# Kernel tuning notes

Measured on AMD Instinct MI355X. Metric: run time of the kernel, lower is better.

## Reference

```python
import jax, jax.numpy as jnp
import numpy as np

B, T, N_EMBD, HEAD = 8, 2048, 1024, 64
NEG_INF = -1e30  # stand-in for float('-inf'), safe under fp16/bf16 after where


def setup_inputs() -> dict:
    key = jax.random.key(0)
    k0, k1, k2, k3 = jax.random.split(key, 4)
    idx = jax.random.normal(k0, (B, T, N_EMBD), dtype=jnp.float32)
    # nn.Linear weights have shape (out_features, in_features)
    Wk = jax.random.normal(k1, (HEAD, N_EMBD), dtype=jnp.float32) * 0.02
    Wq = jax.random.normal(k2, (HEAD, N_EMBD), dtype=jnp.float32) * 0.02
    Wv = jax.random.normal(k3, (HEAD, N_EMBD), dtype=jnp.float32) * 0.02
    return {"idx": idx, "Wk": Wk, "Wq": Wq, "Wv": Wv}


def reference(idx, Wk, Wq, Wv):
    # idx: [B,T,C]; W*: [H,C] (torch Linear layout, y = x @ W.T)
    Tn = idx.shape[1]
    k = jnp.einsum('btc,hc->bth', idx, Wk)
    q = jnp.einsum('btc,hc->bth', idx, Wq)
    v = jnp.einsum('btc,hc->bth', idx, Wv)
    # NOTE: original has NO 1/sqrt(head_size) scaling
    wei = jnp.einsum('bth,bsh->bts', q, k)  # [B,T,T]
    causal = jnp.tril(jnp.ones((Tn, Tn), dtype=bool))  # keep where tril != 0
    wei = jnp.where(causal[None, :, :], wei, NEG_INF)
    # NOTE: original softmaxes over dim=1 (query axis), not the last axis
    wei = jax.nn.softmax(wei, axis=1)
    out = jnp.einsum('bts,bsh->bth', wei, v)  # [B,T,H]
    return out
```

## Files before the change

kernel.cpp:

```cpp
#include <hip/hip_runtime.h>


typedef __attribute__((ext_vector_type(8))) short bf16x8;
typedef __attribute__((ext_vector_type(4))) float f32x4;
typedef unsigned short u16;

#define MFMA(a, b, c) __builtin_amdgcn_mfma_f32_16x16x32_bf16((a), (b), (c), 0, 0, 0)

__device__ __forceinline__ u16 f2bf(float x) {
    unsigned u = __float_as_uint(x);
    u += 0x7fff + ((u >> 16) & 1);
    return (u16)(u >> 16);
}
__device__ __forceinline__ float bf2f(u16 h) {
    return __uint_as_float(((unsigned)h) << 16);
}

#define WH_OFF 0u
#define WL_OFF (WH_OFF + 192u*1024u*2u)
#define QH_OFF (WL_OFF + 192u*1024u*2u)
#define QL_OFF (QH_OFF + 8u*2048u*64u*2u)
#define KH_OFF (QL_OFF + 8u*2048u*64u*2u)
#define KL_OFF (KH_OFF + 8u*2048u*64u*2u)
#define VT_OFF (KL_OFF + 8u*2048u*64u*2u)
#define DD_OFF (VT_OFF + 8u*2048u*64u*2u)

__global__ __launch_bounds__(128) void wsplit_kernel(
    const float* __restrict__ Wk, const float* __restrict__ Wq,
    const float* __restrict__ Wv, u16* __restrict__ FWH, u16* __restrict__ FWL)
{
    const int n = blockIdx.x;
    const int nblk = n >> 4, lr = n & 15;
    const float* src = (n < 64) ? (Wq + (long)n * 1024)
                     : (n < 128) ? (Wk + (long)(n - 64) * 1024)
                                 : (Wv + (long)(n - 128) * 1024);
    const int f = threadIdx.x;
    const int kc = f >> 2, q = f & 3;
    const float4 f0 = *(const float4*)&src[kc * 32 + q * 8];
    const float4 f1 = *(const float4*)&src[kc * 32 + q * 8 + 4];
    const float vs[8] = {f0.x, f0.y, f0.z, f0.w, f1.x, f1.y, f1.z, f1.w};
    bf16x8 hv, lv;
    #pragma unroll
    for (int j = 0; j < 8; ++j) {
        const u16 h = f2bf(vs[j]);
        hv[j] = (short)h;
        lv[j] = (short)f2bf(vs[j] - bf2f(h));
    }
    const long o = ((long)(nblk * 32 + kc) * 64 + q * 16 + lr) * 8;
    *(bf16x8*)&FWH[o] = hv;
    *(bf16x8*)&FWL[o] = lv;
}

__global__ __launch_bounds__(512, 2) void qkv_kernel(
    const float* __restrict__ idx, const u16* __restrict__ FWH, const u16* __restrict__ FWL,
    u16* __restrict__ QH, u16* __restrict__ QL,
    u16* __restrict__ KH, u16* __restrict__ KL, u16* __restrict__ VT)
{
    __shared__ u16 a_l[2][64 * 136];
    const int tid = threadIdx.x;
    const int w = tid >> 6, lr = tid & 15, quad = (tid >> 4) & 3;
    const int lane = tid & 63;
    const int r0 = blockIdx.x * 64;
    const int b = r0 >> 11, t0 = r0 & 2047;
    const int m0 = (w & 1) * 32;
    const int nbb = (w >> 1) * 3;
    const int sr = tid >> 3, sc = (tid & 7) * 8;
    const float* arow = &idx[(long)(r0 + sr) * 1024 + sc];

    f32x4 acc[2][3] = {};
    float4 pf0, pf1;

    pf0 = *(const float4*)(arow);
    pf1 = *(const float4*)(arow + 4);
    {
        const float vs[8] = {pf0.x, pf0.y, pf0.z, pf0.w, pf1.x, pf1.y, pf1.z, pf1.w};
        bf16x8 hv, lv;
        #pragma unroll
        for (int j = 0; j < 8; ++j) {
            const u16 h = f2bf(vs[j]);
            hv[j] = (short)h;
            lv[j] = (short)f2bf(vs[j] - bf2f(h));
        }
        *(bf16x8*)&a_l[0][sr * 136 + sc]      = hv;
        *(bf16x8*)&a_l[0][sr * 136 + 64 + sc] = lv;
    }
    __syncthreads();

    int p = 0;
    for (int it = 0; it < 16; ++it) {
        const int c0 = it * 64;
        if (it < 15) {
            pf0 = *(const float4*)(arow + c0 + 64);
            pf1 = *(const float4*)(arow + c0 + 68);
        }

        bf16x8 AH[2][2], AL[2][2];
        #pragma unroll
        for (int mi = 0; mi < 2; ++mi) {
            const int ar = (m0 + mi * 16 + lr) * 136 + quad * 8;
            AH[mi][0] = *(const bf16x8*)&a_l[p][ar];
            AH[mi][1] = *(const bf16x8*)&a_l[p][ar + 32];
            AL[mi][0] = *(const bf16x8*)&a_l[p][ar + 64];
            AL[mi][1] = *(const bf16x8*)&a_l[p][ar + 96];
        }

        #pragma unroll
        for (int nf = 0; nf < 3; ++nf) {
            const long base = ((long)((nbb + nf) * 32 + 2 * it) * 64 + lane) * 8;
            const bf16x8 bh0 = *(const bf16x8*)&FWH[base];
            const bf16x8 bh1 = *(const bf16x8*)&FWH[base + 512];
            const bf16x8 bl0 = *(const bf16x8*)&FWL[base];
            const bf16x8 bl1 = *(const bf16x8*)&FWL[base + 512];
            #pragma unroll
            for (int mi = 0; mi < 2; ++mi) {
                f32x4 c = acc[mi][nf];
                c = MFMA(AH[mi][0], bh0, c);
                c = MFMA(AL[mi][0], bh0, c);
                c = MFMA(AH[mi][0], bl0, c);
                c = MFMA(AH[mi][1], bh1, c);
                c = MFMA(AL[mi][1], bh1, c);
                c = MFMA(AH[mi][1], bl1, c);
                acc[mi][nf] = c;
            }
        }

        if (it < 15) {
            const float vs[8] = {pf0.x, pf0.y, pf0.z, pf0.w, pf1.x, pf1.y, pf1.z, pf1.w};
            bf16x8 hv, lv;
            #pragma unroll
            for (int j = 0; j < 8; ++j) {
                const u16 h = f2bf(vs[j]);
                hv[j] = (short)h;
                lv[j] = (short)f2bf(vs[j] - bf2f(h));
            }
            *(bf16x8*)&a_l[p ^ 1][sr * 136 + sc]      = hv;
            *(bf16x8*)&a_l[p ^ 1][sr * 136 + 64 + sc] = lv;
            __syncthreads();
            p ^= 1;
        }
    }

    #pragma unroll
    for (int mi = 0; mi < 2; ++mi) {
        const int tb = t0 + m0 + mi * 16 + quad * 4;
        #pragma unroll
        for (int nf = 0; nf < 3; ++nf) {
            const int n = (nbb + nf) * 16 + lr;
            const f32x4 a = acc[mi][nf];
            if (n < 128) {
                u16* Hd = (n < 64) ? QH : KH;
                u16* Ld = (n < 64) ? QL : KL;
                const int h = n & 63;
                #pragma unroll
                for (int r = 0; r < 4; ++r) {
                    const float v = a[r];
                    const u16 hi = f2bf(v);
                    const u16 lo = f2bf(v - bf2f(hi));
                    const long o = (long)(b * 2048 + tb + r) * 64 + h;
                    Hd[o] = hi; Ld[o] = lo;
                }
            } else {
                *(ushort4*)&VT[(long)(b * 64 + n - 128) * 2048 + tb] =
                    make_ushort4(f2bf(a[0]), f2bf(a[1]), f2bf(a[2]), f2bf(a[3]));
            }
        }
    }
}

__global__ __launch_bounds__(256) void stats_kernel(
    const u16* __restrict__ QH, const u16* __restrict__ QL,
    const u16* __restrict__ KH, const u16* __restrict__ KL,
    float* __restrict__ D)
{
    __shared__ u16 kt[64 * 136];
    __shared__ u16 qt[64 * 136];
    __shared__ float red[4][64];
    const int tid = threadIdx.x;
    const int w = tid >> 6, lr = tid & 15, quad = (tid >> 4) & 3;
    const int b = blockIdx.y;
    int x = blockIdx.x, i = 0;
    for (;;) { const int nc = (39 - i) >> 3; if (x < nc) break; x -= nc; ++i; }
    const int c = x;
    const int s0 = i * 64;

    #pragma unroll
    for (int it = 0; it < 2; ++it) {
        const int e = it * 256 + tid;
        const int s = e >> 3, c8 = e & 7;
        const long g = (long)(b * 2048 + s0 + s) * 64 + 8 * c8;
        *(float4*)&kt[s * 136 + 8 * c8]      = *(const float4*)&KH[g];
        *(float4*)&kt[s * 136 + 64 + 8 * c8] = *(const float4*)&KL[g];
    }

    float dsum[4] = {0.f, 0.f, 0.f, 0.f};
    const int ar = (w * 16 + lr) * 136;
    const int jt1 = min(i + 8 * c + 8, 32);
    for (int jt = i + 8 * c; jt < jt1; ++jt) {
        __syncthreads();
        #pragma unroll
        for (int it = 0; it < 2; ++it) {
            const int e = it * 256 + tid;
            const int t = e >> 3, c8 = e & 7;
            const long g = (long)(b * 2048 + jt * 64 + t) * 64 + 8 * c8;
            *(float4*)&qt[t * 136 + 8 * c8]      = *(const float4*)&QH[g];
            *(float4*)&qt[t * 136 + 64 + 8 * c8] = *(const float4*)&QL[g];
        }
        __syncthreads();

        const bf16x8 ah0 = *(const bf16x8*)&qt[ar + quad * 8];
        const bf16x8 al0 = *(const bf16x8*)&qt[ar + 64 + quad * 8];
        const bf16x8 ah1 = *(const bf16x8*)&qt[ar + 32 + quad * 8];
        const bf16x8 al1 = *(const bf16x8*)&qt[ar + 96 + quad * 8];
        #pragma unroll
        for (int nf = 0; nf < 4; ++nf) {
            const int br = (nf * 16 + lr) * 136;
            f32x4 cc = {};
            const bf16x8 bh0 = *(const bf16x8*)&kt[br + quad * 8];
            const bf16x8 bl0 = *(const bf16x8*)&kt[br + 64 + quad * 8];
            cc = MFMA(ah0, bh0, cc); cc = MFMA(ah0, bl0, cc); cc = MFMA(al0, bh0, cc);
            const bf16x8 bh1 = *(const bf16x8*)&kt[br + 32 + quad * 8];
            const bf16x8 bl1 = *(const bf16x8*)&kt[br + 96 + quad * 8];
            cc = MFMA(ah1, bh1, cc); cc = MFMA(ah1, bl1, cc); cc = MFMA(al1, bh1, cc);

            if (jt > i) {
                dsum[nf] += __expf(cc[0]) + __expf(cc[1]) + __expf(cc[2]) + __expf(cc[3]);
            } else {
                const int sl = nf * 16 + lr;
                #pragma unroll
                for (int r = 0; r < 4; ++r) {
                    const int tl = w * 16 + quad * 4 + r;
                    if (tl >= sl) dsum[nf] += __expf(cc[r]);
                }
            }
        }
    }

    #pragma unroll
    for (int nf = 0; nf < 4; ++nf) {
        dsum[nf] += __shfl_xor(dsum[nf], 16);
        dsum[nf] += __shfl_xor(dsum[nf], 32);
    }
    if (quad == 0) {
        #pragma unroll
        for (int nf = 0; nf < 4; ++nf) red[w][nf * 16 + lr] = dsum[nf];
    }
    __syncthreads();
    if (tid < 64)
        atomicAdd(&D[b * 2048 + s0 + tid],
                  red[0][tid] + red[1][tid] + red[2][tid] + red[3][tid]);
}

__global__ __launch_bounds__(256) void out_kernel(
    const u16* __restrict__ QH, const u16* __restrict__ QL,
    const u16* __restrict__ KH, const u16* __restrict__ KL,
    const u16* __restrict__ VT, const float* __restrict__ D,
    float* __restrict__ out)
{
    __shared__ u16 qt[64 * 136];
    __shared__ u16 kt[64 * 136];
    __shared__ u16 vt[64 * 72];
    __shared__ u16 wa[64 * 72];
    __shared__ float rdt[64];
    const int tid = threadIdx.x;
    const int w = tid >> 6, lr = tid & 15, quad = (tid >> 4) & 3;
    const int b = blockIdx.y;
    int x = blockIdx.x, i = 0;
    for (;;) { const int nc = (i + 8) >> 3; if (x < nc) break; x -= nc; ++i; }
    const int c = x;
    const int t0 = i * 64;

    #pragma unroll
    for (int it = 0; it < 2; ++it) {
        const int e = it * 256 + tid;
        const int t = e >> 3, c8 = e & 7;
        const long g = (long)(b * 2048 + t0 + t) * 64 + 8 * c8;
        *(float4*)&qt[t * 136 + 8 * c8]      = *(const float4*)&QH[g];
        *(float4*)&qt[t * 136 + 64 + 8 * c8] = *(const float4*)&QL[g];
    }

    f32x4 oacc[4] = {};
    const int ar = (w * 16 + lr) * 136;
    const int js1 = min(8 * c + 8, i + 1);
    for (int js = 8 * c; js < js1; ++js) {
        const int s0 = js * 64;
        __syncthreads();
        #pragma unroll
        for (int it = 0; it < 2; ++it) {
            const int e = it * 256 + tid;
            const int s = e >> 3, c8 = e & 7;
            const long g = (long)(b * 2048 + s0 + s) * 64 + 8 * c8;
            *(float4*)&kt[s * 136 + 8 * c8]      = *(const float4*)&KH[g];
            *(float4*)&kt[s * 136 + 64 + 8 * c8] = *(const float4*)&KL[g];
        }
        #pragma unroll
        for (int it = 0; it < 2; ++it) {
            const int e = it * 256 + tid;
            const int h = e >> 3, c8 = e & 7;
            *(float4*)&vt[h * 72 + 8 * c8] =
                *(const float4*)&VT[(long)(b * 64 + h) * 2048 + s0 + 8 * c8];
        }
        if (tid < 64) rdt[tid] = 1.0f / D[b * 2048 + s0 + tid];
        __syncthreads();

        const bf16x8 ah0 = *(const bf16x8*)&qt[ar + quad * 8];
        const bf16x8 al0 = *(const bf16x8*)&qt[ar + 64 + quad * 8];
        const bf16x8 ah1 = *(const bf16x8*)&qt[ar + 32 + quad * 8];
        const bf16x8 al1 = *(const bf16x8*)&qt[ar + 96 + quad * 8];
        const bool diag = (js == i);
        #pragma unroll
        for (int nf = 0; nf < 4; ++nf) {
            const int br = (nf * 16 + lr) * 136;
            f32x4 cc = {};
            const bf16x8 bh0 = *(const bf16x8*)&kt[br + quad * 8];
            const bf16x8 bl0 = *(const bf16x8*)&kt[br + 64 + quad * 8];
            cc = MFMA(ah0, bh0, cc); cc = MFMA(ah0, bl0, cc); cc = MFMA(al0, bh0, cc);
            const bf16x8 bh1 = *(const bf16x8*)&kt[br + 32 + quad * 8];
            const bf16x8 bl1 = *(const bf16x8*)&kt[br + 96 + quad * 8];
            cc = MFMA(ah1, bh1, cc); cc = MFMA(ah1, bl1, cc); cc = MFMA(al1, bh1, cc);

            const int sl = nf * 16 + lr;
            const float rv = rdt[sl];
            #pragma unroll
            for (int r = 0; r < 4; ++r) {
                const int tl = w * 16 + quad * 4 + r;
                float wgt = __expf(cc[r]) * rv;
                if (diag && tl < sl) wgt = 0.f;
                wa[tl * 72 + sl] = f2bf(wgt);
            }
        }
        #pragma unroll
        for (int kk = 0; kk < 2; ++kk) {
            const bf16x8 av = *(const bf16x8*)&wa[(w * 16 + lr) * 72 + kk * 32 + quad * 8];
            #pragma unroll
            for (int nf = 0; nf < 4; ++nf) {
                const bf16x8 bv = *(const bf16x8*)&vt[(nf * 16 + lr) * 72 + kk * 32 + quad * 8];
                oacc[nf] = MFMA(av, bv, oacc[nf]);
            }
        }
    }

    const bool single = (i < 8);
    #pragma unroll
    for (int nf = 0; nf < 4; ++nf) {
        const int h = nf * 16 + lr;
        #pragma unroll
        for (int r = 0; r < 4; ++r) {
            const int t = t0 + w * 16 + quad * 4 + r;
            const long o = (long)(b * 2048 + t) * 64 + h;
            if (single) out[o] = oacc[nf][r];
            else        atomicAdd(&out[o], oacc[nf][r]);
        }
    }
}

extern "C" void kernel_launch(void* const* d_in, const int* in_sizes, int n_in,
                              void* d_out, int out_size, void* d_ws, size_t ws_size,
                              hipStream_t stream)
{
    const float* idx = (const float*)d_in[0];
    const float* Wk  = (const float*)d_in[1];
    const float* Wq  = (const float*)d_in[2];
    const float* Wv  = (const float*)d_in[3];
    char* ws = (char*)d_ws;
    float* out = (float*)d_out;

    u16* FWH = (u16*)(ws + WH_OFF); u16* FWL = (u16*)(ws + WL_OFF);
    u16* QH = (u16*)(ws + QH_OFF); u16* QL = (u16*)(ws + QL_OFF);
    u16* KH = (u16*)(ws + KH_OFF); u16* KL = (u16*)(ws + KL_OFF);
    u16* VT = (u16*)(ws + VT_OFF);
    float* Dp = (float*)(ws + DD_OFF);

    hipMemsetAsync(out, 0, (size_t)8 * 2048 * 64 * sizeof(float), stream);
    hipMemsetAsync(Dp, 0, (size_t)8 * 2048 * sizeof(float), stream);

    wsplit_kernel<<<192, 128, 0, stream>>>(Wk, Wq, Wv, FWH, FWL);
    qkv_kernel<<<256, 512, 0, stream>>>(idx, FWH, FWL, QH, QL, KH, KL, VT);
    stats_kernel<<<dim3(80, 8), 256, 0, stream>>>(QH, QL, KH, KL, Dp);
    out_kernel<<<dim3(80, 8), 256, 0, stream>>>(QH, QL, KH, KL, VT, Dp, out);
}
```

Baseline: 169.3 us.

## Store Q/K/V in MFMA fragment layout and load operands directly from global

The QKV projection now writes Q, K (hi/lo) and V in a pre-swizzled MFMA fragment order, so the stats and output kernels can load each lane's bf16x8 operand straight from global memory into registers. This drops most of the shared-memory staging tiles and the block-wide barriers around them. The column chunk per block is halved (4 tiles instead of 8), giving 144 blocks per batch instead of 80, with launch bounds set for 4 blocks per CU. The trade-offs are more atomic adds on the output, scattered 2-byte stores in the projection epilogue, and redundant global reads that now rely on the cache instead of shared-memory reuse.

```diff
diff --git a/kernel.cpp b/kernel.cpp
--- a/kernel.cpp
+++ b/kernel.cpp
@@ -16,14 +16,14 @@
     return __uint_as_float(((unsigned)h) << 16);
 }
 
-#define WH_OFF 0u
-#define WL_OFF (WH_OFF + 192u*1024u*2u)
-#define QH_OFF (WL_OFF + 192u*1024u*2u)
-#define QL_OFF (QH_OFF + 8u*2048u*64u*2u)
-#define KH_OFF (QL_OFF + 8u*2048u*64u*2u)
-#define KL_OFF (KH_OFF + 8u*2048u*64u*2u)
-#define VT_OFF (KL_OFF + 8u*2048u*64u*2u)
-#define DD_OFF (VT_OFF + 8u*2048u*64u*2u)
+#define WH_OFF  0u
+#define WL_OFF  (WH_OFF + 192u*1024u*2u)
+#define FQH_OFF (WL_OFF + 192u*1024u*2u)
+#define FQL_OFF (FQH_OFF + 2u*1024u*1024u)
+#define FKH_OFF (FQL_OFF + 2u*1024u*1024u)
+#define FKL_OFF (FKH_OFF + 2u*1024u*1024u)
+#define VF_OFF  (FKL_OFF + 2u*1024u*1024u)
+#define DD_OFF  (VF_OFF + 2u*1024u*1024u)
 
 __global__ __launch_bounds__(128) void wsplit_kernel(
     const float* __restrict__ Wk, const float* __restrict__ Wq,
@@ -53,8 +53,8 @@
 
 __global__ __launch_bounds__(512, 2) void qkv_kernel(
     const float* __restrict__ idx, const u16* __restrict__ FWH, const u16* __restrict__ FWL,
-    u16* __restrict__ QH, u16* __restrict__ QL,
-    u16* __restrict__ KH, u16* __restrict__ KL, u16* __restrict__ VT)
+    u16* __restrict__ FQH, u16* __restrict__ FQL,
+    u16* __restrict__ FKH, u16* __restrict__ FKL, u16* __restrict__ VF)
 {
     __shared__ u16 a_l[2][64 * 136];
     const int tid = threadIdx.x;
@@ -143,84 +143,82 @@
     #pragma unroll
     for (int mi = 0; mi < 2; ++mi) {
         const int tb = t0 + m0 + mi * 16 + quad * 4;
+        const int tblk = (t0 + m0 + mi * 16) >> 4;
         #pragma unroll
         for (int nf = 0; nf < 3; ++nf) {
             const int n = (nbb + nf) * 16 + lr;
             const f32x4 a = acc[mi][nf];
             if (n < 128) {
-                u16* Hd = (n < 64) ? QH : KH;
-                u16* Ld = (n < 64) ? QL : KL;
+                u16* Hd = (n < 64) ? FQH : FKH;
+                u16* Ld = (n < 64) ? FQL : FKL;
                 const int h = n & 63;
+                const int kc = h >> 5;
+                const int lsub = 16 * ((h & 31) >> 3);
+                const long base = ((long)(b * 128 + tblk) * 2 + kc) * 512 + (h & 7);
                 #pragma unroll
                 for (int r = 0; r < 4; ++r) {
                     const float v = a[r];
                     const u16 hi = f2bf(v);
                     const u16 lo = f2bf(v - bf2f(hi));
-                    const long o = (long)(b * 2048 + tb + r) * 64 + h;
+                    const long o = base + (long)(quad * 4 + r + lsub) * 8;
                     Hd[o] = hi; Ld[o] = lo;
                 }
             } else {
-                *(ushort4*)&VT[(long)(b * 64 + n - 128) * 2048 + tb] =
-                    make_ushort4(f2bf(a[0]), f2bf(a[1]), f2bf(a[2]), f2bf(a[3]));
-            }
-        }
-    }
-}
-
-__global__ __launch_bounds__(256) void stats_kernel(
-    const u16* __restrict__ QH, const u16* __restrict__ QL,
-    const u16* __restrict__ KH, const u16* __restrict__ KL,
+                const int h = n - 128;
+                const int hblk = h >> 4;
+                #pragma unroll
+                for (int r = 0; r < 4; ++r) {
+                    const int t = tb + r;
+                    const long o = ((long)(b * 4 + hblk) * 64 + (t >> 5)) * 512
+                                 + (long)(16 * ((t & 31) >> 3) + (h & 15)) * 8 + (t & 7);
+                    VF[o] = f2bf(a[r]);
+                }
+            }
+        }
+    }
+}
+
+__global__ __launch_bounds__(256, 4) void stats_kernel(
+    const u16* __restrict__ FQH, const u16* __restrict__ FQL,
+    const u16* __restrict__ FKH, const u16* __restrict__ FKL,
     float* __restrict__ D)
 {
-    __shared__ u16 kt[64 * 136];
-    __shared__ u16 qt[64 * 136];
     __shared__ float red[4][64];
     const int tid = threadIdx.x;
     const int w = tid >> 6, lr = tid & 15, quad = (tid >> 4) & 3;
+    const int lane = tid & 63;
     const int b = blockIdx.y;
     int x = blockIdx.x, i = 0;
-    for (;;) { const int nc = (39 - i) >> 3; if (x < nc) break; x -= nc; ++i; }
-    const int c = x;
+    for (;;) { const int nc = (35 - i) >> 2; if (x < nc) break; x -= nc; ++i; }
     const int s0 = i * 64;
-
-    #pragma unroll
-    for (int it = 0; it < 2; ++it) {
-        const int e = it * 256 + tid;
-        const int s = e >> 3, c8 = e & 7;
-        const long g = (long)(b * 2048 + s0 + s) * 64 + 8 * c8;
-        *(float4*)&kt[s * 136 + 8 * c8]      = *(const float4*)&KH[g];
-        *(float4*)&kt[s * 136 + 64 + 8 * c8] = *(const float4*)&KL[g];
+    const int jt0 = i + 4 * x, jt1 = min(jt0 + 4, 32);
+
+    bf16x8 BH[4][2], BL[4][2];
+    #pragma unroll
+    for (int nf = 0; nf < 4; ++nf) {
+        const long kb = ((long)(b * 128 + i * 4 + nf) * 2) * 512 + lane * 8;
+        BH[nf][0] = *(const bf16x8*)&FKH[kb];
+        BH[nf][1] = *(const bf16x8*)&FKH[kb + 512];
+        BL[nf][0] = *(const bf16x8*)&FKL[kb];
+        BL[nf][1] = *(const bf16x8*)&FKL[kb + 512];
     }
 
     float dsum[4] = {0.f, 0.f, 0.f, 0.f};
-    const int ar = (w * 16 + lr) * 136;
-    const int jt1 = min(i + 8 * c + 8, 32);
-    for (int jt = i + 8 * c; jt < jt1; ++jt) {
-        __syncthreads();
-        #pragma unroll
-        for (int it = 0; it < 2; ++it) {
-            const int e = it * 256 + tid;
-            const int t = e >> 3, c8 = e & 7;
-            const long g = (long)(b * 2048 + jt * 64 + t) * 64 + 8 * c8;
-            *(float4*)&qt[t * 136 + 8 * c8]      = *(const float4*)&QH[g];
-            *(float4*)&qt[t * 136 + 64 + 8 * c8] = *(const float4*)&QL[g];
-        }
-        __syncthreads();
-
-        const bf16x8 ah0 = *(const bf16x8*)&qt[ar + quad * 8];
-        const bf16x8 al0 = *(const bf16x8*)&qt[ar + 64 + quad * 8];
-        const bf16x8 ah1 = *(const bf16x8*)&qt[ar + 32 + quad * 8];
-        const bf16x8 al1 = *(const bf16x8*)&qt[ar + 96 + quad * 8];
+    for (int jt = jt0; jt < jt1; ++jt) {
+        const long qb = ((long)(b * 128 + jt * 4 + w) * 2) * 512 + lane * 8;
+        const bf16x8 ah0 = *(const bf16x8*)&FQH[qb];
+        const bf16x8 ah1 = *(const bf16x8*)&FQH[qb + 512];
+        const bf16x8 al0 = *(const bf16x8*)&FQL[qb];
+        const bf16x8 al1 = *(const bf16x8*)&FQL[qb + 512];
         #pragma unroll
         for (int nf = 0; nf < 4; ++nf) {
-            const int br = (nf * 16 + lr) * 136;
             f32x4 cc = {};
-            const bf16x8 bh0 = *(const bf16x8*)&kt[br + quad * 8];
-            const bf16x8 bl0 = *(const bf16x8*)&kt[br + 64 + quad * 8];
-            cc = MFMA(ah0, bh0, cc); cc = MFMA(ah0, bl0, cc); cc = MFMA(al0, bh0, cc);
-            const bf16x8 bh1 = *(const bf16x8*)&kt[br + 32 + quad * 8];
-            const bf16x8 bl1 = *(const bf16x8*)&kt[br + 96 + quad * 8];
-            cc = MFMA(ah1, bh1, cc); cc = MFMA(ah1, bl1, cc); cc = MFMA(al1, bh1, cc);
+            cc = MFMA(ah0, BH[nf][0], cc);
+            cc = MFMA(al0, BH[nf][0], cc);
+            cc = MFMA(ah0, BL[nf][0], cc);
+            cc = MFMA(ah1, BH[nf][1], cc);
+            cc = MFMA(al1, BH[nf][1], cc);
+            cc = MFMA(ah1, BL[nf][1], cc);
 
             if (jt > i) {
                 dsum[nf] += __expf(cc[0]) + __expf(cc[1]) + __expf(cc[2]) + __expf(cc[3]);
@@ -250,96 +248,84 @@
                   red[0][tid] + red[1][tid] + red[2][tid] + red[3][tid]);
 }
 
-__global__ __launch_bounds__(256) void out_kernel(
-    const u16* __restrict__ QH, const u16* __restrict__ QL,
-    const u16* __restrict__ KH, const u16* __restrict__ KL,
-    const u16* __restrict__ VT, const float* __restrict__ D,
+__global__ __launch_bounds__(256, 4) void out_kernel(
+    const u16* __restrict__ FQH, const u16* __restrict__ FQL,
+    const u16* __restrict__ FKH, const u16* __restrict__ FKL,
+    const u16* __restrict__ VF, const float* __restrict__ D,
     float* __restrict__ out)
 {
-    __shared__ u16 qt[64 * 136];
-    __shared__ u16 kt[64 * 136];
-    __shared__ u16 vt[64 * 72];
     __shared__ u16 wa[64 * 72];
-    __shared__ float rdt[64];
     const int tid = threadIdx.x;
     const int w = tid >> 6, lr = tid & 15, quad = (tid >> 4) & 3;
+    const int lane = tid & 63;
     const int b = blockIdx.y;
     int x = blockIdx.x, i = 0;
-    for (;;) { const int nc = (i + 8) >> 3; if (x < nc) break; x -= nc; ++i; }
-    const int c = x;
+    for (;;) { const int nc = (i + 4) >> 2; if (x < nc) break; x -= nc; ++i; }
     const int t0 = i * 64;
-
-    #pragma unroll
-    for (int it = 0; it < 2; ++it) {
-        const int e = it * 256 + tid;
-        const int t = e >> 3, c8 = e & 7;
-        const long g = (long)(b * 2048 + t0 + t) * 64 + 8 * c8;
-        *(float4*)&qt[t * 136 + 8 * c8]      = *(const float4*)&QH[g];
-        *(float4*)&qt[t * 136 + 64 + 8 * c8] = *(const float4*)&QL[g];
-    }
+    const int js0 = 4 * x, js1 = min(4 * x + 4, i + 1);
+
+    const long qb = ((long)(b * 128 + i * 4 + w) * 2) * 512 + lane * 8;
+    const bf16x8 qh0 = *(const bf16x8*)&FQH[qb];
+    const bf16x8 qh1 = *(const bf16x8*)&FQH[qb + 512];
+    const bf16x8 ql0 = *(const bf16x8*)&FQL[qb];
+    const bf16x8 ql1 = *(const bf16x8*)&FQL[qb + 512];
 
     f32x4 oacc[4] = {};
-    const int ar = (w * 16 + lr) * 136;
-    const int js1 = min(8 * c + 8, i + 1);
-    for (int js = 8 * c; js < js1; ++js) {
+    for (int js = js0; js < js1; ++js) {
         const int s0 = js * 64;
-        __syncthreads();
-        #pragma unroll
-        for (int it = 0; it < 2; ++it) {
-            const int e = it * 256 + tid;
-            const int s = e >> 3, c8 = e & 7;
-            const long g = (long)(b * 2048 + s0 + s) * 64 + 8 * c8;
-            *(float4*)&kt[s * 136 + 8 * c8]      = *(const float4*)&KH[g];
-            *(float4*)&kt[s * 136 + 64 + 8 * c8] = *(const float4*)&KL[g];
-        }
-        #pragma unroll
-        for (int it = 0; it < 2; ++it) {
-            const int e = it * 256 + tid;
-            const int h = e >> 3, c8 = e & 7;
-            *(float4*)&vt[h * 72 + 8 * c8] =
-                *(const float4*)&VT[(long)(b * 64 + h) * 2048 + s0 + 8 * c8];
-        }
-        if (tid < 64) rdt[tid] = 1.0f / D[b * 2048 + s0 + tid];
-        __syncthreads();
-
-        const bf16x8 ah0 = *(const bf16x8*)&qt[ar + quad * 8];
-        const bf16x8 al0 = *(const bf16x8*)&qt[ar + 64 + quad * 8];
-        const bf16x8 ah1 = *(const bf16x8*)&qt[ar + 32 + quad * 8];
-        const bf16x8 al1 = *(const bf16x8*)&qt[ar + 96 + quad * 8];
         const bool diag = (js == i);
+
+        f32x4 cc[4];
+        float rv[4];
         #pragma unroll
         for (int nf = 0; nf < 4; ++nf) {
-            const int br = (nf * 16 + lr) * 136;
-            f32x4 cc = {};
-            const bf16x8 bh0 = *(const bf16x8*)&kt[br + quad * 8];
-            const bf16x8 bl0 = *(const bf16x8*)&kt[br + 64 + quad * 8];
-            cc = MFMA(ah0, bh0, cc); cc = MFMA(ah0, bl0, cc); cc = MFMA(al0, bh0, cc);
-            const bf16x8 bh1 = *(const bf16x8*)&kt[br + 32 + quad * 8];
-            const bf16x8 bl1 = *(const bf16x8*)&kt[br + 96 + quad * 8];
-            cc = MFMA(ah1, bh1, cc); cc = MFMA(ah1, bl1, cc); cc = MFMA(al1, bh1, cc);
-
+            const long kb = ((long)(b * 128 + js * 4 + nf) * 2) * 512 + lane * 8;
+            const bf16x8 bh0 = *(const bf16x8*)&FKH[kb];
+            const bf16x8 bh1 = *(const bf16x8*)&FKH[kb + 512];
+            const bf16x8 bl0 = *(const bf16x8*)&FKL[kb];
+            const bf16x8 bl1 = *(const bf16x8*)&FKL[kb + 512];
+            rv[nf] = D[b * 2048 + s0 + nf * 16 + lr];
+            f32x4 c = {};
+            c = MFMA(qh0, bh0, c);
+            c = MFMA(ql0, bh0, c);
+            c = MFMA(qh0, bl0, c);
+            c = MFMA(qh1, bh1, c);
+            c = MFMA(ql1, bh1, c);
+            c = MFMA(qh1, bl1, c);
+            cc[nf] = c;
+        }
+
+        bf16x8 VB[4][2];
+        #pragma unroll
+        for (int nf = 0; nf < 4; ++nf) {
+            const long vb = ((long)(b * 4 + nf) * 64 + 2 * js) * 512 + lane * 8;
+            VB[nf][0] = *(const bf16x8*)&VF[vb];
+            VB[nf][1] = *(const bf16x8*)&VF[vb + 512];
+        }
+
+        #pragma unroll
+        for (int nf = 0; nf < 4; ++nf) {
             const int sl = nf * 16 + lr;
-            const float rv = rdt[sl];
+            const float r_ = 1.0f / rv[nf];
             #pragma unroll
             for (int r = 0; r < 4; ++r) {
                 const int tl = w * 16 + quad * 4 + r;
-                float wgt = __expf(cc[r]) * rv;
-                if (diag && tl < sl) wgt = 0.f;
-                wa[tl * 72 + sl] = f2bf(wgt);
-            }
-        }
+                float pv = __expf(cc[nf][r]) * r_;
+                if (diag && tl < sl) pv = 0.f;
+                wa[tl * 72 + sl] = f2bf(pv);
+            }
+        }
+
         #pragma unroll
         for (int kk = 0; kk < 2; ++kk) {
             const bf16x8 av = *(const bf16x8*)&wa[(w * 16 + lr) * 72 + kk * 32 + quad * 8];
             #pragma unroll
-            for (int nf = 0; nf < 4; ++nf) {
-                const bf16x8 bv = *(const bf16x8*)&vt[(nf * 16 + lr) * 72 + kk * 32 + quad * 8];
-                oacc[nf] = MFMA(av, bv, oacc[nf]);
-            }
-        }
-    }
-
-    const bool single = (i < 8);
+            for (int nf = 0; nf < 4; ++nf)
+                oacc[nf] = MFMA(av, VB[nf][kk], oacc[nf]);
+        }
+    }
+
+    const bool single = (i < 4);
     #pragma unroll
     for (int nf = 0; nf < 4; ++nf) {
         const int h = nf * 16 + lr;
@@ -364,17 +350,17 @@
     char* ws = (char*)d_ws;
     float* out = (float*)d_out;
 
-    u16* FWH = (u16*)(ws + WH_OFF); u16* FWL = (u16*)(ws + WL_OFF);
-    u16* QH = (u16*)(ws + QH_OFF); u16* QL = (u16*)(ws + QL_OFF);
-    u16* KH = (u16*)(ws + KH_OFF); u16* KL = (u16*)(ws + KL_OFF);
-    u16* VT = (u16*)(ws + VT_OFF);
+    u16* FWH = (u16*)(ws + WH_OFF);  u16* FWL = (u16*)(ws + WL_OFF);
+    u16* FQH = (u16*)(ws + FQH_OFF); u16* FQL = (u16*)(ws + FQL_OFF);
+    u16* FKH = (u16*)(ws + FKH_OFF); u16* FKL = (u16*)(ws + FKL_OFF);
+    u16* VF  = (u16*)(ws + VF_OFF);
     float* Dp = (float*)(ws + DD_OFF);
 
     hipMemsetAsync(out, 0, (size_t)8 * 2048 * 64 * sizeof(float), stream);
     hipMemsetAsync(Dp, 0, (size_t)8 * 2048 * sizeof(float), stream);
 
     wsplit_kernel<<<192, 128, 0, stream>>>(Wk, Wq, Wv, FWH, FWL);
-    qkv_kernel<<<256, 512, 0, stream>>>(idx, FWH, FWL, QH, QL, KH, KL, VT);
-    stats_kernel<<<dim3(80, 8), 256, 0, stream>>>(QH, QL, KH, KL, Dp);
-    out_kernel<<<dim3(80, 8), 256, 0, stream>>>(QH, QL, KH, KL, VT, Dp, out);
-}
+    qkv_kernel<<<256, 512, 0, stream>>>(idx, FWH, FWL, FQH, FQL, FKH, FKL, VF);
+    stats_kernel<<<dim3(144, 8), 256, 0, stream>>>(FQH, FQL, FKH, FKL, Dp);
+    out_kernel<<<dim3(144, 8), 256, 0, stream>>>(FQH, FQL, FKH, FKL, VF, Dp, out);
+}
```

After: 173.0 us. 2.2% more time.
